# Kernel optimization log

Hardware: AMD Instinct MI355X
Metric: run time of the kernel (lower is better)

## Reference

```python
import jax, jax.numpy as jnp
import numpy as np

D_MODEL = 1024
NUM_HEADS = 16
D_K = D_MODEL // NUM_HEADS


def setup_inputs() -> dict:
    key = jax.random.key(0)
    ks = jax.random.split(key, 5)
    s = 1.0 / np.sqrt(D_MODEL)
    return {
        "x": jax.random.normal(ks[0], (2, 2048, D_MODEL), dtype=jnp.float32),
        "Wq": jax.random.normal(ks[1], (D_MODEL, D_MODEL), dtype=jnp.float32) * s,
        "bq": jnp.zeros((D_MODEL,), dtype=jnp.float32),
        "Wk": jax.random.normal(ks[2], (D_MODEL, D_MODEL), dtype=jnp.float32) * s,
        "bk": jnp.zeros((D_MODEL,), dtype=jnp.float32),
        "Wv": jax.random.normal(ks[3], (D_MODEL, D_MODEL), dtype=jnp.float32) * s,
        "bv": jnp.zeros((D_MODEL,), dtype=jnp.float32),
        "Wo": jax.random.normal(ks[4], (D_MODEL, D_MODEL), dtype=jnp.float32) * s,
        "bo": jnp.zeros((D_MODEL,), dtype=jnp.float32),
    }


def reference(x, Wq, bq, Wk, bk, Wv, bv, Wo, bo):
    B, S, D = x.shape
    H, dk = NUM_HEADS, D_K
    Q = x @ Wq + bq  # [B, S, D]
    K = x @ Wk + bk
    V = x @ Wv + bv
    # Faithful to the torch code: plain .view(B, H, S, dk) (NO transpose),
    # i.e. heads are carved out of the flattened (S*D) dim, not the feature dim.
    Q = Q.reshape(B, H, S, dk)
    K = K.reshape(B, H, S, dk)
    V = V.reshape(B, H, S, dk)
    scores = jnp.einsum("bhqd,bhkd->bhqk", Q, K) / jnp.sqrt(jnp.float32(dk))
    attn = jax.nn.softmax(scores, axis=-1)  # [B, H, S, S]
    ctx = jnp.einsum("bhqk,bhkd->bhqd", attn, V)  # [B, H, S, dk]
    out = ctx.reshape(B, S, D) @ Wo + bo
    return out  # dropout is identity in eval mode
```

## Files before the change

### kernel.cpp

```cpp
#include <hip/hip_runtime.h>
#include <hip/hip_bf16.h>
#include <math.h>

#define D_MODEL 1024
#define SEQ     2048
#define BATCH   2
#define NHEAD   16
#define DKH     64
#define BH      (BATCH * NHEAD)

typedef unsigned short u16;
typedef unsigned int   u32;
typedef __bf16 bf16x8 __attribute__((ext_vector_type(8)));
typedef float  f32x4  __attribute__((ext_vector_type(4)));

#define MFMA16(a, b, c) __builtin_amdgcn_mfma_f32_16x16x32_bf16((a), (b), (c), 0, 0, 0)
#define AS1 __attribute__((address_space(1)))
#define AS3 __attribute__((address_space(3)))

#define QSCALE 0.18033688f

__device__ __forceinline__ u16 f2bf(float x) {
    u32 u = __float_as_uint(x);
    u += 0x7fffu + ((u >> 16) & 1u);
    return (u16)(u >> 16);
}
__device__ __forceinline__ float bf2f(u16 b) {
    return __uint_as_float(((u32)b) << 16);
}
__device__ __forceinline__ void gl16(const u16* g, void* lds) {
    __builtin_amdgcn_global_load_lds((const AS1 u32*)g, (AS3 u32*)lds, 16, 0, 0);
}

__global__ __launch_bounds__(256) void conv_all(
    const float* __restrict__ x, u16* __restrict__ Xh, int n4,
    const float* __restrict__ W0, const float* __restrict__ W1,
    const float* __restrict__ W2, const float* __restrict__ W3,
    u16* __restrict__ H0, u16* __restrict__ L0, u16* __restrict__ H1, u16* __restrict__ L1,
    u16* __restrict__ H2, u16* __restrict__ L2, u16* __restrict__ H3, u16* __restrict__ L3)
{
    const int t = threadIdx.x;
    if ((int)blockIdx.x < 4096) {
        int i = blockIdx.x * 256 + t;
        if (i >= n4) return;
        float4 v = reinterpret_cast<const float4*>(x)[i];
        uint2 H;
        H.x = f2bf(v.x) | ((u32)f2bf(v.y) << 16);
        H.y = f2bf(v.z) | ((u32)f2bf(v.w) << 16);
        reinterpret_cast<uint2*>(Xh)[i] = H;
        return;
    }
    int id = blockIdx.x - 4096;
    int bx = id & 15, by = (id >> 4) & 15, bz = id >> 8;
    const float* W; u16 *Ht, *Lt;
    if (bz == 0)      { W = W0; Ht = H0; Lt = L0; }
    else if (bz == 1) { W = W1; Ht = H1; Lt = L1; }
    else if (bz == 2) { W = W2; Ht = H2; Lt = L2; }
    else              { W = W3; Ht = H3; Lt = L3; }

    __shared__ float T[64][65];
    const int n0 = bx * 64, k0 = by * 64;
    #pragma unroll
    for (int i = 0; i < 4; ++i) {
        int f = t + i * 256;
        int kr = f >> 4, ns = (f & 15) * 4;
        float4 v = *reinterpret_cast<const float4*>(&W[(size_t)(k0 + kr) * D_MODEL + n0 + ns]);
        T[kr][ns + 0] = v.x; T[kr][ns + 1] = v.y; T[kr][ns + 2] = v.z; T[kr][ns + 3] = v.w;
    }
    __syncthreads();
    #pragma unroll
    for (int i = 0; i < 4; ++i) {
        int f = t + i * 256;
        int nr = f >> 4, ks = (f & 15) * 4;
        u16 hh[4], ll[4];
        #pragma unroll
        for (int j = 0; j < 4; ++j) {
            float xv = T[ks + j][nr];
            u16 hb = f2bf(xv);
            hh[j] = hb;
            ll[j] = f2bf(xv - bf2f(hb));
        }
        uint2 H, L;
        H.x = hh[0] | ((u32)hh[1] << 16); H.y = hh[2] | ((u32)hh[3] << 16);
        L.x = ll[0] | ((u32)ll[1] << 16); L.y = ll[2] | ((u32)ll[3] << 16);
        size_t o = (size_t)(n0 + nr) * D_MODEL + k0 + ks;
        *reinterpret_cast<uint2*>(&Ht[o]) = H;
        *reinterpret_cast<uint2*>(&Lt[o]) = L;
    }
}

__global__ __launch_bounds__(512, 2) void gemm_qkv(
    const u16* __restrict__ AhG,
    const u16* __restrict__ Bqh, const u16* __restrict__ Bql,
    const u16* __restrict__ Bkh, const u16* __restrict__ Bkl,
    const u16* __restrict__ Bvh, const u16* __restrict__ Bvl,
    const float* __restrict__ bq, const float* __restrict__ bk, const float* __restrict__ bv,
    u16* __restrict__ Qb, u16* __restrict__ Kb, u16* __restrict__ Vb)
{
    constexpr int K = D_MODEL, N = D_MODEL;
    __shared__ u16 LB[2][28672];

    const int tid  = threadIdx.x;
    const int wv   = tid >> 6;
    const int lane = tid & 63;
    const int quad = lane >> 4;
    const int l16  = lane & 15;
    const int wm   = wv & 1, wn = wv >> 1;
    const int brow = blockIdx.y * 128, bcol = blockIdx.x * 128;

    const u16* sp[7];
    int sldb[7];
    #pragma unroll
    for (int j = 0; j < 7; ++j) {
        int c = wv * 7 + j, a = c >> 3, cc = c & 7;
        int row = cc * 16 + (lane >> 2);
        int gseg = (lane & 3) ^ ((lane >> 3) & 3);
        const u16* p;
        if (a == 0)      p = AhG;
        else if (a == 1) p = Bqh;
        else if (a == 2) p = Bql;
        else if (a == 3) p = Bkh;
        else if (a == 4) p = Bkl;
        else if (a == 5) p = Bvh;
        else             p = Bvl;
        int rbase = (a == 0) ? brow : bcol;
        sp[j]   = p + (size_t)(rbase + row) * K + gseg * 8;
        sldb[j] = a * 8192 + cc * 1024;
    }

    int aro[4], bro[2];
    #pragma unroll
    for (int i = 0; i < 4; ++i) {
        int mr = wm * 64 + i * 16 + l16;
        aro[i] = mr * 64 + ((quad ^ ((mr >> 1) & 3)) * 16);
    }
    #pragma unroll
    for (int i = 0; i < 2; ++i) {
        int nr = wn * 32 + i * 16 + l16;
        bro[i] = nr * 64 + ((quad ^ ((nr >> 1) & 3)) * 16);
    }

    f32x4 acc[3][4][2] = {};

    #pragma unroll
    for (int j = 0; j < 7; ++j)
        gl16(sp[j], (char*)LB[0] + sldb[j]);

    for (int it = 0; it < K / 32; ++it) {
        const int cur = it & 1;
        __syncthreads();
        if (it + 1 < K / 32) {
            const int nxt = cur ^ 1;
            const int k1 = (it + 1) * 32;
            #pragma unroll
            for (int j = 0; j < 7; ++j)
                gl16(sp[j] + k1, (char*)LB[nxt] + sldb[j]);
        }

        bf16x8 ah[4];
        #pragma unroll
        for (int i = 0; i < 4; ++i)
            ah[i] = *reinterpret_cast<const bf16x8*>((const char*)LB[cur] + aro[i]);
        #pragma unroll
        for (int m = 0; m < 3; ++m) {
            const int bbh = (1 + 2 * m) * 8192, bbl = (2 + 2 * m) * 8192;
            bf16x8 bh[2], bl[2];
            #pragma unroll
            for (int i = 0; i < 2; ++i) {
                bh[i] = *reinterpret_cast<const bf16x8*>((const char*)LB[cur] + bbh + bro[i]);
                bl[i] = *reinterpret_cast<const bf16x8*>((const char*)LB[cur] + bbl + bro[i]);
            }
            #pragma unroll
            for (int mi = 0; mi < 4; ++mi)
                #pragma unroll
                for (int ni = 0; ni < 2; ++ni) {
                    f32x4 c = acc[m][mi][ni];
                    c = MFMA16(ah[mi], bh[ni], c);
                    c = MFMA16(ah[mi], bl[ni], c);
                    acc[m][mi][ni] = c;
                }
        }
    }

    #pragma unroll
    for (int m = 0; m < 3; ++m) {
        const float* bias = (m == 0) ? bq : (m == 1) ? bk : bv;
        u16* out = (m == 0) ? Qb : (m == 1) ? Kb : Vb;
        const float sc = (m == 0) ? QSCALE : 1.0f;
        #pragma unroll
        for (int mi = 0; mi < 4; ++mi) {
            #pragma unroll
            for (int ni = 0; ni < 2; ++ni) {
                int col = bcol + wn * 32 + ni * 16 + l16;
                float bvv = bias[col];
                #pragma unroll
                for (int r = 0; r < 4; ++r) {
                    int row = brow + wm * 64 + mi * 16 + quad * 4 + r;
                    out[(size_t)row * N + col] = f2bf((acc[m][mi][ni][r] + bvv) * sc);
                }
            }
        }
    }
}

__global__ __launch_bounds__(512, 2) void gemm_oproj(
    const u16* __restrict__ AhG, const u16* __restrict__ Bh, const u16* __restrict__ Bl,
    const float* __restrict__ bias, float* __restrict__ Cf)
{
    constexpr int K = D_MODEL, N = D_MODEL;
    __shared__ u16 LB[2][12288];

    const int tid  = threadIdx.x;
    const int wv   = tid >> 6;
    const int lane = tid & 63;
    const int quad = lane >> 4;
    const int l16  = lane & 15;
    const int wm   = wv & 1, wn = wv >> 1;
    const int brow = blockIdx.y * 128, bcol = blockIdx.x * 128;

    const u16* sp[3];
    int sldb[3];
    #pragma unroll
    for (int j = 0; j < 3; ++j) {
        int c = wv * 3 + j, a = c >> 3, cc = c & 7;
        int row = cc * 16 + (lane >> 2);
        int gseg = (lane & 3) ^ ((lane >> 3) & 3);
        const u16* p = (a == 0) ? AhG : (a == 1) ? Bh : Bl;
        int rbase = (a == 0) ? brow : bcol;
        sp[j]   = p + (size_t)(rbase + row) * K + gseg * 8;
        sldb[j] = a * 8192 + cc * 1024;
    }

    int aro[4], bro[2];
    #pragma unroll
    for (int i = 0; i < 4; ++i) {
        int mr = wm * 64 + i * 16 + l16;
        aro[i] = mr * 64 + ((quad ^ ((mr >> 1) & 3)) * 16);
    }
    #pragma unroll
    for (int i = 0; i < 2; ++i) {
        int nr = wn * 32 + i * 16 + l16;
        bro[i] = nr * 64 + ((quad ^ ((nr >> 1) & 3)) * 16);
    }

    f32x4 acc[4][2] = {};

    #pragma unroll
    for (int j = 0; j < 3; ++j)
        gl16(sp[j], (char*)LB[0] + sldb[j]);

    for (int it = 0; it < K / 32; ++it) {
        const int cur = it & 1;
        __syncthreads();
        if (it + 1 < K / 32) {
            const int nxt = cur ^ 1;
            const int k1 = (it + 1) * 32;
            #pragma unroll
            for (int j = 0; j < 3; ++j)
                gl16(sp[j] + k1, (char*)LB[nxt] + sldb[j]);
        }

        bf16x8 ah[4], bh[2], bl[2];
        #pragma unroll
        for (int i = 0; i < 4; ++i)
            ah[i] = *reinterpret_cast<const bf16x8*>((const char*)LB[cur] + aro[i]);
        #pragma unroll
        for (int i = 0; i < 2; ++i) {
            bh[i] = *reinterpret_cast<const bf16x8*>((const char*)LB[cur] + 8192 + bro[i]);
            bl[i] = *reinterpret_cast<const bf16x8*>((const char*)LB[cur] + 16384 + bro[i]);
        }
        #pragma unroll
        for (int mi = 0; mi < 4; ++mi)
            #pragma unroll
            for (int ni = 0; ni < 2; ++ni) {
                f32x4 c = acc[mi][ni];
                c = MFMA16(ah[mi], bh[ni], c);
                c = MFMA16(ah[mi], bl[ni], c);
                acc[mi][ni] = c;
            }
    }

    #pragma unroll
    for (int mi = 0; mi < 4; ++mi) {
        #pragma unroll
        for (int ni = 0; ni < 2; ++ni) {
            int col = bcol + wn * 32 + ni * 16 + l16;
            float bvv = bias[col];
            #pragma unroll
            for (int r = 0; r < 4; ++r) {
                int row = brow + wm * 64 + mi * 16 + quad * 4 + r;
                Cf[(size_t)row * N + col] = acc[mi][ni][r] + bvv;
            }
        }
    }
}

__global__ __launch_bounds__(256) void v_transpose(
    const u16* __restrict__ V, u16* __restrict__ Vt)
{
    __shared__ u16 T[64][72];
    const int bh = blockIdx.y, st = blockIdx.x;
    const u16* src = V + ((size_t)bh * SEQ + (size_t)st * 64) * 64;
    const int t = threadIdx.x;
    #pragma unroll
    for (int i = 0; i < 2; ++i) {
        int c  = t + i * 256;
        int s  = c >> 3;
        int d0 = (c & 7) * 8;
        uint4 v = reinterpret_cast<const uint4*>(src)[c];
        u16 e[8];
        e[0] = (u16)(v.x & 0xffff); e[1] = (u16)(v.x >> 16);
        e[2] = (u16)(v.y & 0xffff); e[3] = (u16)(v.y >> 16);
        e[4] = (u16)(v.z & 0xffff); e[5] = (u16)(v.z >> 16);
        e[6] = (u16)(v.w & 0xffff); e[7] = (u16)(v.w >> 16);
        #pragma unroll
        for (int j = 0; j < 8; ++j) T[d0 + j][s] = e[j];
    }
    __syncthreads();
    const int d = t >> 2, seg = t & 3;
    u16* dst = Vt + (size_t)bh * 64 * SEQ + (size_t)d * SEQ + st * 64 + seg * 16;
    uint4 a = *reinterpret_cast<const uint4*>(&T[d][seg * 16]);
    uint4 b = *reinterpret_cast<const uint4*>(&T[d][seg * 16 + 8]);
    reinterpret_cast<uint4*>(dst)[0] = a;
    reinterpret_cast<uint4*>(dst)[1] = b;
}

__global__ __launch_bounds__(256, 2) void attn_mfma(
    const u16* __restrict__ Qb_g, const u16* __restrict__ Kb_g,
    const u16* __restrict__ Vt_g, u16* __restrict__ Ch_g)
{
    __shared__ u16 KVS[3][8192];
    __shared__ u16 Pb [128 * 72];

    const int tid  = threadIdx.x;
    const int wv   = tid >> 6;
    const int lane = tid & 63;
    const int quad = lane >> 4;
    const int l16  = lane & 15;
    const int id   = blockIdx.x;
    const int bh   = id & 31;
    const int qt   = id >> 5;

    const size_t qbase = ((size_t)bh * SEQ + (size_t)qt * 128) * 64;
    const size_t kbh   = (size_t)bh * SEQ * 64;
    const size_t vtbh  = (size_t)bh * 64 * SEQ;

    bf16x8 qf[2][2];
    #pragma unroll
    for (int sub = 0; sub < 2; ++sub)
        #pragma unroll
        for (int ks = 0; ks < 2; ++ks) {
            size_t o = qbase + (size_t)(wv * 32 + sub * 16 + l16) * 64 + ks * 32 + quad * 8;
            qf[sub][ks] = *reinterpret_cast<const bf16x8*>(Qb_g + o);
        }

    const u16* sp[4];
    size_t sstep[4];
    int sldb[4];
    #pragma unroll
    for (int j = 0; j < 4; ++j) {
        int c   = wv * 4 + j;
        int arr = c >> 3, cc = c & 7;
        int row = cc * 8 + (lane >> 3);
        int sg  = (lane & 7) ^ (row & 7);
        if (arr == 0) { sp[j] = Kb_g + kbh + (size_t)row * 64 + sg * 8;   sstep[j] = 4096; }
        else          { sp[j] = Vt_g + vtbh + (size_t)row * SEQ + sg * 8; sstep[j] = 64; }
        sldb[j] = arr * 8192 + cc * 1024;
    }

    int fro[4][2];
    #pragma unroll
    for (int t = 0; t < 4; ++t)
        #pragma unroll
        for (int ks = 0; ks < 2; ++ks)
            fro[t][ks] = (t * 16 + l16) * 128 + (((ks * 4 + quad) ^ (l16 & 7)) * 16);

    bf16x8 onesv;
    #pragma unroll
    for (int i = 0; i < 8; ++i) onesv[i] = (__bf16)1.0f;

    f32x4 oacc[2][4] = {};
    f32x4 lsum[2] = {};

    auto S_step = [&](int bufidx, f32x4 (&sacc)[2][4]) {
        const char* kb = (const char*)KVS[bufidx];
        #pragma unroll
        for (int t4 = 0; t4 < 4; ++t4) {
            bf16x8 kh0 = *reinterpret_cast<const bf16x8*>(kb + fro[t4][0]);
            bf16x8 kh1 = *reinterpret_cast<const bf16x8*>(kb + fro[t4][1]);
            #pragma unroll
            for (int sub = 0; sub < 2; ++sub) {
                f32x4 a = sacc[sub][t4];
                a = MFMA16(qf[sub][0], kh0, a);
                a = MFMA16(qf[sub][1], kh1, a);
                sacc[sub][t4] = a;
            }
        }
    };

    auto PV_step = [&](int bufidx) {
        const char* vb = (const char*)KVS[bufidx] + 8192;
        bf16x8 bvf[4][2];
        #pragma unroll
        for (int dt = 0; dt < 4; ++dt) {
            bvf[dt][0] = *reinterpret_cast<const bf16x8*>(vb + fro[dt][0]);
            bvf[dt][1] = *reinterpret_cast<const bf16x8*>(vb + fro[dt][1]);
        }
        #pragma unroll
        for (int sub = 0; sub < 2; ++sub) {
            bf16x8 ap[2];
            #pragma unroll
            for (int ks = 0; ks < 2; ++ks)
                ap[ks] = *reinterpret_cast<const bf16x8*>(
                    &Pb[(wv * 32 + sub * 16 + l16) * 72 + ks * 32 + quad * 8]);
            #pragma unroll
            for (int dt = 0; dt < 4; ++dt) {
                oacc[sub][dt] = MFMA16(ap[0], bvf[dt][0], oacc[sub][dt]);
                oacc[sub][dt] = MFMA16(ap[1], bvf[dt][1], oacc[sub][dt]);
            }
            lsum[sub] = MFMA16(ap[0], onesv, lsum[sub]);
            lsum[sub] = MFMA16(ap[1], onesv, lsum[sub]);
        }
    };

    auto EXP2_step = [&](f32x4 (&sacc)[2][4]) {
        #pragma unroll
        for (int sub = 0; sub < 2; ++sub) {
            int rowb = wv * 32 + sub * 16 + quad * 4;
            #pragma unroll
            for (int r = 0; r < 4; ++r) {
                u32 u0 = __float_as_uint(__builtin_amdgcn_exp2f(sacc[sub][0][r]));
                u32 u1 = __float_as_uint(__builtin_amdgcn_exp2f(sacc[sub][1][r]));
                u32 u2 = __float_as_uint(__builtin_amdgcn_exp2f(sacc[sub][2][r]));
                u32 u3 = __float_as_uint(__builtin_amdgcn_exp2f(sacc[sub][3][r]));
                int ro = (rowb + r) * 72 + l16;
                Pb[ro +  0] = (u16)(u0 >> 16);
                Pb[ro + 16] = (u16)(u1 >> 16);
                Pb[ro + 32] = (u16)(u2 >> 16);
                Pb[ro + 48] = (u16)(u3 >> 16);
            }
        }
    };

    #pragma unroll
    for (int j = 0; j < 4; ++j)
        gl16(sp[j], (char*)KVS[0] + sldb[j]);

    {
        __syncthreads();
        #pragma unroll
        for (int j = 0; j < 4; ++j)
            gl16(sp[j] + sstep[j], (char*)KVS[1] + sldb[j]);
        f32x4 sacc[2][4] = {};
        __builtin_amdgcn_s_setprio(1);
        S_step(0, sacc);
        __builtin_amdgcn_s_setprio(0);
        EXP2_step(sacc);
    }

    int cur = 1, prv = 0, nxt = 2;
    for (int kt = 1; kt < SEQ / 64; ++kt) {
        __syncthreads();
        if (kt + 1 < SEQ / 64) {
            #pragma unroll
            for (int j = 0; j < 4; ++j)
                gl16(sp[j] + (size_t)(kt + 1) * sstep[j], (char*)KVS[nxt] + sldb[j]);
        }

        f32x4 sacc[2][4] = {};
        __builtin_amdgcn_s_setprio(1);
        S_step(cur, sacc);
        PV_step(prv);
        __builtin_amdgcn_s_setprio(0);
        EXP2_step(sacc);

        prv = cur; cur = nxt; nxt = (nxt == 2) ? 0 : nxt + 1;
    }

    __builtin_amdgcn_s_setprio(1);
    PV_step(prv);
    __builtin_amdgcn_s_setprio(0);

    u16* Oh = Ch_g + qbase;
    #pragma unroll
    for (int sub = 0; sub < 2; ++sub) {
        float inv[4];
        #pragma unroll
        for (int r = 0; r < 4; ++r) inv[r] = 1.0f / lsum[sub][r];
        #pragma unroll
        for (int dt = 0; dt < 4; ++dt)
            #pragma unroll
            for (int r = 0; r < 4; ++r) {
                int row = wv * 32 + sub * 16 + quad * 4 + r;
                Oh[(size_t)row * 64 + dt * 16 + l16] = f2bf(oacc[sub][dt][r] * inv[r]);
            }
    }
}

extern "C" void kernel_launch(void* const* d_in, const int* in_sizes, int n_in,
                              void* d_out, int out_size, void* d_ws, size_t ws_size,
                              hipStream_t stream)
{
    const float* x  = (const float*)d_in[0];
    const float* Wq = (const float*)d_in[1];
    const float* bq = (const float*)d_in[2];
    const float* Wk = (const float*)d_in[3];
    const float* bk = (const float*)d_in[4];
    const float* Wv = (const float*)d_in[5];
    const float* bv = (const float*)d_in[6];
    const float* Wo = (const float*)d_in[7];
    const float* bo = (const float*)d_in[8];
    float* out = (float*)d_out;

    const int M = BATCH * SEQ;
    const int N = D_MODEL;
    const size_t NE = (size_t)M * N;
    const size_t NW = (size_t)N * N;

    u16* w16 = (u16*)d_ws;
    u16* Xh   = w16;
    u16* Qb   = Xh   + NE;
    u16* Kb   = Qb   + NE;
    u16* Vb   = Kb   + NE;
    u16* Vtb  = Vb   + NE;
    u16* Ctxh = Vtb  + NE;
    u16* WTqh = Ctxh + NE;
    u16* WTql = WTqh + NW;
    u16* WTkh = WTql + NW;
    u16* WTkl = WTkh + NW;
    u16* WTvh = WTkl + NW;
    u16* WTvl = WTvh + NW;
    u16* WToh = WTvl + NW;
    u16* WTol = WToh + NW;

    conv_all<<<dim3(4096 + 1024), dim3(256), 0, stream>>>(
        x, Xh, (int)(NE / 4),
        Wq, Wk, Wv, Wo, WTqh, WTql, WTkh, WTkl, WTvh, WTvl, WToh, WTol);

    gemm_qkv<<<dim3(N / 128, M / 128), dim3(512), 0, stream>>>(
        Xh, WTqh, WTql, WTkh, WTkl, WTvh, WTvl, bq, bk, bv, Qb, Kb, Vb);

    v_transpose<<<dim3(SEQ / 64, BH), dim3(256), 0, stream>>>(Vb, Vtb);

    attn_mfma<<<dim3((SEQ / 128) * BH), dim3(256), 0, stream>>>(Qb, Kb, Vtb, Ctxh);

    gemm_oproj<<<dim3(N / 128, M / 128), dim3(512), 0, stream>>>(
        Ctxh, WToh, WTol, bo, out);
}
```

Before: 218.5 us.

## Stage QKV projection GEMM loads per matrix with partial waitcnt barriers

Reorders the per-wave global-to-LDS load assignments so the A tile plus each of the Q, K and V weight halves land in separate groups. The main loop is split into three phases, each waiting only on the loads it needs (partial vmcnt) before a barrier, then issuing the next tile's loads for that group. MFMA blocks are wrapped in raised wave priority, and the last iteration is peeled. This aims to overlap global loads with MFMA work at a finer grain than one full-tile barrier. It adds more barriers per iteration and depends on correct hand-counted vmcnt values.

After: 212.8 us. -2.6%, faster.

```diff
diff --git a/kernel.cpp b/kernel.cpp
--- a/kernel.cpp
+++ b/kernel.cpp
@@ -112,7 +112,10 @@
     int sldb[7];
     #pragma unroll
     for (int j = 0; j < 7; ++j) {
-        int c = wv * 7 + j, a = c >> 3, cc = c & 7;
+        int c = (j < 3) ? (wv * 3 + j)
+              : (j < 5) ? (24 + wv * 2 + (j - 3))
+                        : (40 + wv * 2 + (j - 5));
+        int a = c >> 3, cc = c & 7;
         int row = cc * 16 + (lane >> 2);
         int gseg = (lane & 3) ^ ((lane >> 3) & 3);
         const u16* p;
@@ -142,44 +145,84 @@
 
     f32x4 acc[3][4][2] = {};
 
+    auto rdB = [&](int cur, int m, bf16x8 (&bh)[2], bf16x8 (&bl)[2]) {
+        const int bbh = (1 + 2 * m) * 8192, bbl = (2 + 2 * m) * 8192;
+        #pragma unroll
+        for (int i = 0; i < 2; ++i) {
+            bh[i] = *reinterpret_cast<const bf16x8*>((const char*)LB[cur] + bbh + bro[i]);
+            bl[i] = *reinterpret_cast<const bf16x8*>((const char*)LB[cur] + bbl + bro[i]);
+        }
+    };
+    auto mm = [&](int m, bf16x8 (&ah)[4], bf16x8 (&bh)[2], bf16x8 (&bl)[2]) {
+        __builtin_amdgcn_s_setprio(1);
+        #pragma unroll
+        for (int mi = 0; mi < 4; ++mi)
+            #pragma unroll
+            for (int ni = 0; ni < 2; ++ni) {
+                f32x4 c = acc[m][mi][ni];
+                c = MFMA16(ah[mi], bh[ni], c);
+                c = MFMA16(ah[mi], bl[ni], c);
+                acc[m][mi][ni] = c;
+            }
+        __builtin_amdgcn_s_setprio(0);
+    };
+
     #pragma unroll
     for (int j = 0; j < 7; ++j)
         gl16(sp[j], (char*)LB[0] + sldb[j]);
 
-    for (int it = 0; it < K / 32; ++it) {
-        const int cur = it & 1;
-        __syncthreads();
-        if (it + 1 < K / 32) {
-            const int nxt = cur ^ 1;
-            const int k1 = (it + 1) * 32;
-            #pragma unroll
-            for (int j = 0; j < 7; ++j)
-                gl16(sp[j] + k1, (char*)LB[nxt] + sldb[j]);
-        }
-
-        bf16x8 ah[4];
+    for (int it = 0; it < K / 32 - 1; ++it) {
+        const int cur = it & 1, nx = cur ^ 1;
+        const int k1 = (it + 1) * 32;
+        bf16x8 ah[4], bh[2], bl[2];
+
+        asm volatile("s_waitcnt vmcnt(4)" ::: "memory");
+        __builtin_amdgcn_s_barrier();
         #pragma unroll
         for (int i = 0; i < 4; ++i)
             ah[i] = *reinterpret_cast<const bf16x8*>((const char*)LB[cur] + aro[i]);
-        #pragma unroll
-        for (int m = 0; m < 3; ++m) {
-            const int bbh = (1 + 2 * m) * 8192, bbl = (2 + 2 * m) * 8192;
-            bf16x8 bh[2], bl[2];
-            #pragma unroll
-            for (int i = 0; i < 2; ++i) {
-                bh[i] = *reinterpret_cast<const bf16x8*>((const char*)LB[cur] + bbh + bro[i]);
-                bl[i] = *reinterpret_cast<const bf16x8*>((const char*)LB[cur] + bbl + bro[i]);
-            }
-            #pragma unroll
-            for (int mi = 0; mi < 4; ++mi)
-                #pragma unroll
-                for (int ni = 0; ni < 2; ++ni) {
-                    f32x4 c = acc[m][mi][ni];
-                    c = MFMA16(ah[mi], bh[ni], c);
-                    c = MFMA16(ah[mi], bl[ni], c);
-                    acc[m][mi][ni] = c;
-                }
-        }
+        rdB(cur, 0, bh, bl);
+        gl16(sp[0] + k1, (char*)LB[nx] + sldb[0]);
+        gl16(sp[1] + k1, (char*)LB[nx] + sldb[1]);
+        gl16(sp[2] + k1, (char*)LB[nx] + sldb[2]);
+        mm(0, ah, bh, bl);
+
+        asm volatile("s_waitcnt vmcnt(5)" ::: "memory");
+        __builtin_amdgcn_s_barrier();
+        rdB(cur, 1, bh, bl);
+        gl16(sp[3] + k1, (char*)LB[nx] + sldb[3]);
+        gl16(sp[4] + k1, (char*)LB[nx] + sldb[4]);
+        mm(1, ah, bh, bl);
+
+        asm volatile("s_waitcnt vmcnt(5)" ::: "memory");
+        __builtin_amdgcn_s_barrier();
+        rdB(cur, 2, bh, bl);
+        gl16(sp[5] + k1, (char*)LB[nx] + sldb[5]);
+        gl16(sp[6] + k1, (char*)LB[nx] + sldb[6]);
+        mm(2, ah, bh, bl);
+    }
+
+    {
+        const int cur = (K / 32 - 1) & 1;
+        bf16x8 ah[4], bh[2], bl[2];
+
+        asm volatile("s_waitcnt vmcnt(4)" ::: "memory");
+        __builtin_amdgcn_s_barrier();
+        #pragma unroll
+        for (int i = 0; i < 4; ++i)
+            ah[i] = *reinterpret_cast<const bf16x8*>((const char*)LB[cur] + aro[i]);
+        rdB(cur, 0, bh, bl);
+        mm(0, ah, bh, bl);
+
+        asm volatile("s_waitcnt vmcnt(2)" ::: "memory");
+        __builtin_amdgcn_s_barrier();
+        rdB(cur, 1, bh, bl);
+        mm(1, ah, bh, bl);
+
+        asm volatile("s_waitcnt vmcnt(0)" ::: "memory");
+        __builtin_amdgcn_s_barrier();
+        rdB(cur, 2, bh, bl);
+        mm(2, ah, bh, bl);
     }
 
     #pragma unroll
```
